# Optimization experiments

Measured on AMD Instinct MI355X. Metric: run time of the kernel, lower is better.

Reference implementation:

```python
import jax, jax.numpy as jnp
import numpy as np

H = 8  # num_heads
NEG = -1e6  # mask fill value used by the torch masked_softmax


def layernorm(x, g, b, eps=1e-5):
    mu = jnp.mean(x, axis=-1, keepdims=True)
    var = jnp.mean(jnp.square(x - mu), axis=-1, keepdims=True)
    return (x - mu) * jax.lax.rsqrt(var + eps) * g + b


def setup_inputs() -> dict:
    key = jax.random.key(0)
    ks = jax.random.split(key, 10)
    B, S, D, F = 8, 1024, 512, 2048
    s = 0.02
    return {
        "X": jax.random.normal(ks[0], (B, S, D), jnp.float32),
        "valid_lens": jax.random.randint(ks[1], (B,), 1, S + 1, jnp.int32),
        "ln1_g": jnp.ones((D,), jnp.float32),
        "ln1_b": jnp.zeros((D,), jnp.float32),
        "Wq": jax.random.normal(ks[2], (D, D), jnp.float32) * s,
        "Wk": jax.random.normal(ks[3], (D, D), jnp.float32) * s,
        "Wv": jax.random.normal(ks[4], (D, D), jnp.float32) * s,
        "Wo": jax.random.normal(ks[5], (D, D), jnp.float32) * s,
        "ln2_g": jnp.ones((D,), jnp.float32),
        "ln2_b": jnp.zeros((D,), jnp.float32),
        "W1": jax.random.normal(ks[6], (D, F), jnp.float32) * s,
        "b1": jnp.zeros((F,), jnp.float32),
        "W2": jax.random.normal(ks[7], (F, D), jnp.float32) * s,
        "b2": jnp.zeros((D,), jnp.float32),
    }


def vit_block(X, valid_lens, ln1_g, ln1_b, Wq, Wk, Wv, Wo, ln2_g, ln2_b, W1, b1, W2, b2):
    B, S, D = X.shape
    dh = D // H
    h = layernorm(X, ln1_g, ln1_b)
    # project and split heads: [B, S, H, dh]
    q = (h @ Wq).reshape(B, S, H, dh)
    k = (h @ Wk).reshape(B, S, H, dh)
    v = (h @ Wv).reshape(B, S, H, dh)
    scores = jnp.einsum("bqhd,bkhd->bhqk", q, k) / jnp.sqrt(jnp.float32(dh))
    # mask keys >= valid_len[b] with -1e6 (as in masked_softmax)
    mask = jnp.arange(S)[None, None, None, :] < valid_lens[:, None, None, None]
    scores = jnp.where(mask, scores, NEG)
    attn = jax.nn.softmax(scores, axis=-1)
    out = jnp.einsum("bhqk,bkhd->bqhd", attn, v).reshape(B, S, D)
    X = X + out @ Wo
    h2 = layernorm(X, ln2_g, ln2_b)
    mlp = jax.nn.gelu(h2 @ W1 + b1, approximate=False) @ W2 + b2
    return X + mlp


def reference(X, valid_lens, ln1_g, ln1_b, Wq, Wk, Wv, Wo, ln2_g, ln2_b, W1, b1, W2, b2):
    return vit_block(X, valid_lens, ln1_g, ln1_b, Wq, Wk, Wv, Wo, ln2_g, ln2_b, W1, b1, W2, b2)
```

## Files before the change

kernel.cpp:

```cpp
#include <hip/hip_runtime.h>
#include <math.h>

#define BB 8
#define SS 1024
#define DD 512
#define FF 2048
#define NH 8
#define MM (BB * SS)
#define LDQKV 1536

using bf8 = __attribute__((ext_vector_type(8))) short;
using f4  = __attribute__((ext_vector_type(4))) float;

#define AS1 __attribute__((address_space(1)))
#define AS3 __attribute__((address_space(3)))

__device__ __forceinline__ void gload16(const void* g, void* l) {
  __builtin_amdgcn_global_load_lds((AS1 const void*)g, (AS3 void*)l, 16, 0, 0);
}

template <int N> __device__ __forceinline__ void wait_vm() {
  if constexpr (N == 0)      asm volatile("s_waitcnt vmcnt(0)" ::: "memory");
  else if constexpr (N == 3) asm volatile("s_waitcnt vmcnt(3)" ::: "memory");
  else if constexpr (N == 4) asm volatile("s_waitcnt vmcnt(4)" ::: "memory");
  else if constexpr (N == 6) asm volatile("s_waitcnt vmcnt(6)" ::: "memory");
  else                       asm volatile("s_waitcnt vmcnt(8)" ::: "memory");
  __builtin_amdgcn_sched_barrier(0);
}

__device__ __forceinline__ void bar() {
  __builtin_amdgcn_sched_barrier(0);
  __builtin_amdgcn_s_barrier();
  __builtin_amdgcn_sched_barrier(0);
}

__device__ __forceinline__ unsigned short f2b(float f) {
  union { float f; unsigned u; } v; v.f = f;
  unsigned r = v.u + 0x7fffu + ((v.u >> 16) & 1u);
  return (unsigned short)(r >> 16);
}

__device__ __forceinline__ float gelu_f(float x) {
  float ax = fabsf(x) * 0.70710678118654752f;
  float t = 1.0f / (1.0f + 0.3275911f * ax);
  float poly = t * (0.254829592f +
               t * (-0.284496736f +
               t * (1.421413741f +
               t * (-1.453152027f + t * 1.061405429f))));
  float erfv = 1.0f - poly * __expf(-ax * ax);
  erfv = copysignf(erfv, x);
  return 0.5f * x * (1.0f + erfv);
}

__global__ __launch_bounds__(256) void ln_bf16(const float* __restrict__ x,
                                               const float* __restrict__ g,
                                               const float* __restrict__ bta,
                                               unsigned short* __restrict__ out) {
  int wave = threadIdx.x >> 6, lane = threadIdx.x & 63;
  int row = (blockIdx.x << 2) + wave;
  const float* xr = x + (size_t)row * DD;
  int base = lane << 3;
  float4 v0 = *(const float4*)(xr + base);
  float4 v1 = *(const float4*)(xr + base + 4);
  float s  = v0.x + v0.y + v0.z + v0.w + v1.x + v1.y + v1.z + v1.w;
  float sq = v0.x*v0.x + v0.y*v0.y + v0.z*v0.z + v0.w*v0.w
           + v1.x*v1.x + v1.y*v1.y + v1.z*v1.z + v1.w*v1.w;
  for (int m = 32; m; m >>= 1) { s += __shfl_xor(s, m); sq += __shfl_xor(sq, m); }
  float mu  = s * (1.0f / DD);
  float var = sq * (1.0f / DD) - mu * mu;
  float rs  = rsqrtf(var + 1e-5f);
  float xv[8], go[8], bo[8];
  *(float4*)(xv) = v0; *(float4*)(xv + 4) = v1;
  *(float4*)(go)     = *(const float4*)(g + base);
  *(float4*)(go + 4) = *(const float4*)(g + base + 4);
  *(float4*)(bo)     = *(const float4*)(bta + base);
  *(float4*)(bo + 4) = *(const float4*)(bta + base + 4);
  union { unsigned short u[8]; uint4 v; } ov;
#pragma unroll
  for (int i = 0; i < 8; i++) ov.u[i] = f2b((xv[i] - mu) * rs * go[i] + bo[i]);
  *(uint4*)(out + (size_t)row * DD + base) = ov.v;
}

__global__ __launch_bounds__(256) void tconv(const float* __restrict__ in,
                                             unsigned short* __restrict__ outp,
                                             int K, int N) {
  __shared__ float tile[32][33];
  int n0 = blockIdx.x << 5, k0 = blockIdx.y << 5;
  int c = threadIdx.x & 31, r = threadIdx.x >> 5;
#pragma unroll
  for (int i = 0; i < 4; i++)
    tile[r + 8 * i][c] = in[(size_t)(k0 + r + 8 * i) * N + n0 + c];
  __syncthreads();
#pragma unroll
  for (int i = 0; i < 4; i++)
    outp[(size_t)(n0 + r + 8 * i) * K + k0 + c] = f2b(tile[c][r + 8 * i]);
}

__global__ __launch_bounds__(256) void tconv4(
    const float* __restrict__ s0, const float* __restrict__ s1,
    const float* __restrict__ s2, const float* __restrict__ s3,
    unsigned short* __restrict__ d0, unsigned short* __restrict__ d1,
    unsigned short* __restrict__ d2, unsigned short* __restrict__ d3) {
  __shared__ float tile[32][33];
  const float* in; unsigned short* outp;
  switch (blockIdx.z) {
    case 0: in = s0; outp = d0; break;
    case 1: in = s1; outp = d1; break;
    case 2: in = s2; outp = d2; break;
    default: in = s3; outp = d3; break;
  }
  int n0 = blockIdx.x << 5, k0 = blockIdx.y << 5;
  int c = threadIdx.x & 31, r = threadIdx.x >> 5;
#pragma unroll
  for (int i = 0; i < 4; i++)
    tile[r + 8 * i][c] = in[(size_t)(k0 + r + 8 * i) * DD + n0 + c];
  __syncthreads();
#pragma unroll
  for (int i = 0; i < 4; i++)
    outp[(size_t)(n0 + r + 8 * i) * DD + k0 + c] = f2b(tile[c][r + 8 * i]);
}

template <int BM, int BN, int ACT>
__global__ __launch_bounds__(256, 4) void gemm_t(
    const unsigned short* __restrict__ A,
    const unsigned short* __restrict__ Bt,
    const float* __restrict__ bias,
    const float* __restrict__ res,
    float* __restrict__ Cf,
    unsigned short* __restrict__ Cb,
    int M, int N, int K, int gx) {
  constexpr int WM = BM / 2, WN = BN / 2;
  constexpr int FM = WM / 16, FN = WN / 16;
  constexpr int ACH = BM / 64, BCH = BN / 64;
  constexpr int L = ACH + BCH;
  __shared__ unsigned short As[2][BM * 32];
  __shared__ unsigned short Bs[2][BN * 32];
  int tid = threadIdx.x, wid = tid >> 6, lane = tid & 63;

  int bid = blockIdx.x;
  int cpx = (int)gridDim.x >> 3;
  int swz = (bid & 7) * cpx + (bid >> 3);
  int m0 = (swz / gx) * BM, n0 = (swz % gx) * BN;

  int wm = (wid >> 1) * WM, wn = (wid & 1) * WN;
  int r4 = lane & 15, ksl = lane >> 4;
  int srow = lane >> 2;
  int gs = (lane & 3) ^ ((lane >> 3) & 3);

  const unsigned short* aBase =
      A + (size_t)(m0 + wid * (ACH * 16) + srow) * K + gs * 8;
  const unsigned short* bBase =
      Bt + (size_t)(n0 + wid * (BCH * 16) + srow) * K + gs * 8;

  f4 acc[FN][FM];
#pragma unroll
  for (int i = 0; i < FN; i++)
#pragma unroll
    for (int j = 0; j < FM; j++) acc[i][j] = (f4){0.f, 0.f, 0.f, 0.f};

  auto STAGE = [&](int buf, int t) {
    int k0 = t << 5;
#pragma unroll
    for (int i = 0; i < ACH; i++)
      gload16(aBase + (size_t)i * 16 * K + k0, &As[buf][(wid * ACH + i) * 512]);
#pragma unroll
    for (int i = 0; i < BCH; i++)
      gload16(bBase + (size_t)i * 16 * K + k0, &Bs[buf][(wid * BCH + i) * 512]);
  };

  auto COMPUTE = [&](int buf) {
    bf8 af[FM], bfr[FN];
#pragma unroll
    for (int mi = 0; mi < FM; mi++) {
      int r = wm + mi * 16 + r4;
      af[mi] = *(const bf8*)((const char*)&As[buf][0] + r * 64 +
                             ((ksl ^ ((r >> 1) & 3)) << 4));
    }
#pragma unroll
    for (int ni = 0; ni < FN; ni++) {
      int r = wn + ni * 16 + r4;
      bfr[ni] = *(const bf8*)((const char*)&Bs[buf][0] + r * 64 +
                              ((ksl ^ ((r >> 1) & 3)) << 4));
    }
#pragma unroll
    for (int ni = 0; ni < FN; ni++)
#pragma unroll
      for (int mi = 0; mi < FM; mi++)
        acc[ni][mi] = __builtin_amdgcn_mfma_f32_16x16x32_bf16(
            bfr[ni], af[mi], acc[ni][mi], 0, 0, 0);
  };

  int nt = K >> 5;
  STAGE(0, 0);
  STAGE(1, 1);
  for (int t = 0; t < nt; t++) {
    if (t + 1 < nt) wait_vm<L>();
    else            wait_vm<0>();
    bar();
    COMPUTE(t & 1);
    bar();
    if (t + 2 < nt) STAGE(t & 1, t + 2);
  }

  int rq = (lane >> 4) << 2;
#pragma unroll
  for (int ni = 0; ni < FN; ni++) {
    int col = n0 + wn + ni * 16 + rq;
    float bv[4] = {0.f, 0.f, 0.f, 0.f};
    if (bias) *(float4*)bv = *(const float4*)(bias + col);
#pragma unroll
    for (int mi = 0; mi < FM; mi++) {
      int row = m0 + wm + mi * 16 + r4;
      float v[4];
#pragma unroll
      for (int j = 0; j < 4; j++) {
        v[j] = acc[ni][mi][j] + bv[j];
        if (ACT) v[j] = gelu_f(v[j]);
      }
      if (res) {
        float4 rv = *(const float4*)(res + (size_t)row * N + col);
        v[0] += rv.x; v[1] += rv.y; v[2] += rv.z; v[3] += rv.w;
      }
      if (Cf) {
        *(float4*)(Cf + (size_t)row * N + col) = *(float4*)v;
      } else {
        union { unsigned short u[4]; uint2 q; } p;
#pragma unroll
        for (int j = 0; j < 4; j++) p.u[j] = f2b(v[j]);
        *(uint2*)(Cb + (size_t)row * N + col) = p.q;
      }
    }
  }
}

__global__ __launch_bounds__(256) void attn_mfma(
    const unsigned short* __restrict__ QKV,
    const int* __restrict__ vlen,
    unsigned short* __restrict__ AO) {
  __shared__ unsigned short Qs[64 * 64];
  __shared__ unsigned short Ks[64 * 64];
  __shared__ unsigned short Vt[64 * 64];
  __shared__ unsigned short Ps[64 * 64];
  int b = blockIdx.z, h = blockIdx.y, q0 = blockIdx.x << 6;
  int tid = threadIdx.x, wid = tid >> 6, lane = tid & 63;
  int vl = vlen[b];
  int r4 = lane & 15, ksl = lane >> 4;

  int srow = lane >> 3;
  int gs = (lane & 7) ^ srow;
  {
    const unsigned short* qsrc =
        QKV + (size_t)(b * SS + q0 + wid * 16 + srow) * LDQKV + h * 64 + gs * 8;
    gload16(qsrc, Qs + wid * 1024);
    gload16(qsrc + (size_t)8 * LDQKV, Qs + wid * 1024 + 512);
  }
  const unsigned short* kbase =
      QKV + (size_t)(b * SS + wid * 16 + srow) * LDQKV + DD + h * 64 + gs * 8;
  int vp = tid & 31, vdg = (tid >> 5) << 3;
  const unsigned short* vbase =
      QKV + (size_t)(b * SS + 2 * vp) * LDQKV + 2 * DD + h * 64 + vdg;

  f4 o[4];
#pragma unroll
  for (int i = 0; i < 4; i++) o[i] = (f4){0.f, 0.f, 0.f, 0.f};
  float mrun[4], lrun[4];
#pragma unroll
  for (int j = 0; j < 4; j++) { mrun[j] = -3e38f; lrun[j] = 0.0f; }

  int ntiles = (vl + 63) >> 6;
  if (ntiles > 16) ntiles = 16;

  for (int t = 0; t < ntiles; t++) {
    int kg0 = t << 6;
    const unsigned short* ks = kbase + (size_t)kg0 * LDQKV;
    gload16(ks, Ks + wid * 1024);
    gload16(ks + (size_t)8 * LDQKV, Ks + wid * 1024 + 512);
    {
      const unsigned short* v0 = vbase + (size_t)kg0 * LDQKV;
      const unsigned short* v1 = v0 + LDQKV;
      unsigned short va[8], vb[8];
      *(uint4*)va = *(const uint4*)v0;
      *(uint4*)vb = *(const uint4*)v1;
#pragma unroll
      for (int i = 0; i < 8; i++) {
        int d = vdg + i;
        unsigned val = (unsigned)va[i] | ((unsigned)vb[i] << 16);
        int byte = (d << 7) + (((vp >> 2) ^ (d & 7)) << 4) + ((vp & 3) << 2);
        *(unsigned*)((char*)Vt + byte) = val;
      }
    }
    __syncthreads();

    f4 s[4];
#pragma unroll
    for (int i = 0; i < 4; i++) s[i] = (f4){0.f, 0.f, 0.f, 0.f};
#pragma unroll
    for (int k2 = 0; k2 < 2; k2++) {
      int slot = (k2 << 2) + ksl;
      int qr = (wid << 4) + r4;
      bf8 aq = *(const bf8*)((const char*)Qs + (qr << 7) + ((slot ^ (qr & 7)) << 4));
#pragma unroll
      for (int ni = 0; ni < 4; ni++) {
        int kr = (ni << 4) + r4;
        bf8 bk = *(const bf8*)((const char*)Ks + (kr << 7) + ((slot ^ (kr & 7)) << 4));
        s[ni] = __builtin_amdgcn_mfma_f32_16x16x32_bf16(aq, bk, s[ni], 0, 0, 0);
      }
    }

#pragma unroll
    for (int j = 0; j < 4; j++) {
      int qr = (wid << 4) + ((lane >> 4) << 2) + j;
      float sv[4], mx = -3e38f;
#pragma unroll
      for (int ni = 0; ni < 4; ni++) {
        float v = s[ni][j] * 0.125f;
        if (kg0 + (ni << 4) + r4 >= vl) v = -1e6f;
        sv[ni] = v;
        mx = fmaxf(mx, v);
      }
#pragma unroll
      for (int m2 = 1; m2 < 16; m2 <<= 1) mx = fmaxf(mx, __shfl_xor(mx, m2));
      float mnew = fmaxf(mrun[j], mx);
      float al = __expf(mrun[j] - mnew);
      float ls = 0.0f;
      unsigned short pb[4];
#pragma unroll
      for (int ni = 0; ni < 4; ni++) {
        float p = __expf(sv[ni] - mnew);
        ls += p;
        pb[ni] = f2b(p);
      }
#pragma unroll
      for (int m2 = 1; m2 < 16; m2 <<= 1) ls += __shfl_xor(ls, m2);
      lrun[j] = lrun[j] * al + ls;
      mrun[j] = mnew;
#pragma unroll
      for (int ni = 0; ni < 4; ni++) {
        int kc = (ni << 4) + r4;
        int byte = (qr << 7) + (((kc >> 3) ^ (qr & 7)) << 4) + ((kc & 7) << 1);
        *(unsigned short*)((char*)Ps + byte) = pb[ni];
        o[ni][j] *= al;
      }
    }

#pragma unroll
    for (int k2 = 0; k2 < 2; k2++) {
      int slot = (k2 << 2) + ksl;
      int qr = (wid << 4) + r4;
      bf8 ap = *(const bf8*)((const char*)Ps + (qr << 7) + ((slot ^ (qr & 7)) << 4));
#pragma unroll
      for (int ni = 0; ni < 4; ni++) {
        int dr = (ni << 4) + r4;
        bf8 bv = *(const bf8*)((const char*)Vt + (dr << 7) + ((slot ^ (dr & 7)) << 4));
        o[ni] = __builtin_amdgcn_mfma_f32_16x16x32_bf16(ap, bv, o[ni], 0, 0, 0);
      }
    }
    __syncthreads();
  }

  float inv[4];
#pragma unroll
  for (int j = 0; j < 4; j++) inv[j] = 1.0f / lrun[j];
#pragma unroll
  for (int ni = 0; ni < 4; ni++) {
#pragma unroll
    for (int j = 0; j < 4; j++) {
      int qr = (wid << 4) + ((lane >> 4) << 2) + j;
      int d = (ni << 4) + r4;
      AO[(size_t)(b * SS + q0 + qr) * DD + h * 64 + d] = f2b(o[ni][j] * inv[j]);
    }
  }
}

extern "C" void kernel_launch(void* const* d_in, const int* in_sizes, int n_in,
                              void* d_out, int out_size, void* d_ws,
                              size_t ws_size, hipStream_t stream) {
  const float* X    = (const float*)d_in[0];
  const int*   vln  = (const int*)d_in[1];
  const float* ln1g = (const float*)d_in[2];
  const float* ln1b = (const float*)d_in[3];
  const float* Wq   = (const float*)d_in[4];
  const float* Wk   = (const float*)d_in[5];
  const float* Wv   = (const float*)d_in[6];
  const float* Wo   = (const float*)d_in[7];
  const float* ln2g = (const float*)d_in[8];
  const float* ln2b = (const float*)d_in[9];
  const float* W1   = (const float*)d_in[10];
  const float* b1   = (const float*)d_in[11];
  const float* W2   = (const float*)d_in[12];
  const float* b2   = (const float*)d_in[13];
  float* out = (float*)d_out;

  unsigned short* ws = (unsigned short*)d_ws;
  unsigned short* h     = ws;
  unsigned short* QKVb  = h     + (size_t)MM * DD;
  unsigned short* AOb   = QKVb  + (size_t)MM * LDQKV;
  unsigned short* mid   = AOb   + (size_t)MM * DD;
  unsigned short* Wqkvt = mid   + (size_t)MM * FF;
  unsigned short* Wot   = Wqkvt + (size_t)3 * DD * DD;
  unsigned short* W1t   = Wot   + (size_t)DD * DD;
  unsigned short* W2t   = W1t   + (size_t)FF * DD;

  dim3 blk(256);

  tconv4<<<dim3(16, 16, 4), blk, 0, stream>>>(
      Wq, Wk, Wv, Wo, Wqkvt, Wqkvt + (size_t)DD * DD,
      Wqkvt + (size_t)2 * DD * DD, Wot);
  tconv<<<dim3(64, 16), blk, 0, stream>>>(W1, W1t, DD, FF);
  tconv<<<dim3(16, 64), blk, 0, stream>>>(W2, W2t, FF, DD);

  ln_bf16<<<dim3(MM / 4), blk, 0, stream>>>(X, ln1g, ln1b, h);
  gemm_t<128, 128, 0><<<dim3((LDQKV / 128) * (MM / 128)), blk, 0, stream>>>(
      h, Wqkvt, nullptr, nullptr, nullptr, QKVb, MM, LDQKV, DD, LDQKV / 128);
  attn_mfma<<<dim3(SS / 64, NH, BB), blk, 0, stream>>>(QKVb, vln, AOb);
  gemm_t<128, 64, 0><<<dim3((DD / 64) * (MM / 128)), blk, 0, stream>>>(
      AOb, Wot, nullptr, X, out, nullptr, MM, DD, DD, DD / 64);
  ln_bf16<<<dim3(MM / 4), blk, 0, stream>>>(out, ln2g, ln2b, h);
  gemm_t<128, 128, 1><<<dim3((FF / 128) * (MM / 128)), blk, 0, stream>>>(
      h, W1t, b1, nullptr, nullptr, mid, MM, FF, DD, FF / 128);
  gemm_t<128, 64, 0><<<dim3((DD / 64) * (MM / 128)), blk, 0, stream>>>(
      mid, W2t, b2, out, out, nullptr, MM, DD, FF, DD / 64);
}
```

Before: 179.4 us.

## Replace GEMM kernel with 512-thread 256-wide tiles and 64-deep K steps

Rewrites the bf16 MFMA GEMM to use 8 waves per block, larger output tiles (256x256 for QKV and W1, 64x256 for the D-output GEMMs) and a K step of 64 with a new 128-byte-row XOR swizzle in LDS. It also raises wave priority around the MFMA section. The goal is more data reuse per LDS load and fewer barriers per K. The trade-offs are more LDS and registers per block, lower occupancy, and fewer blocks in the grid (for example 192 for QKV), which may underfill the CUs. The epilogue changes from vectorized float4 stores to scalar per-element stores with a transposed accumulator mapping, which may reduce store coalescing.

```diff
diff --git a/kernel.cpp b/kernel.cpp
--- a/kernel.cpp
+++ b/kernel.cpp
@@ -21,10 +21,9 @@
 
 template <int N> __device__ __forceinline__ void wait_vm() {
   if constexpr (N == 0)      asm volatile("s_waitcnt vmcnt(0)" ::: "memory");
-  else if constexpr (N == 3) asm volatile("s_waitcnt vmcnt(3)" ::: "memory");
-  else if constexpr (N == 4) asm volatile("s_waitcnt vmcnt(4)" ::: "memory");
-  else if constexpr (N == 6) asm volatile("s_waitcnt vmcnt(6)" ::: "memory");
-  else                       asm volatile("s_waitcnt vmcnt(8)" ::: "memory");
+  else if constexpr (N == 5) asm volatile("s_waitcnt vmcnt(5)" ::: "memory");
+  else if constexpr (N == 8) asm volatile("s_waitcnt vmcnt(8)" ::: "memory");
+  else                       asm volatile("s_waitcnt vmcnt(16)" ::: "memory");
   __builtin_amdgcn_sched_barrier(0);
 }
 
@@ -120,8 +119,8 @@
     outp[(size_t)(n0 + r + 8 * i) * DD + k0 + c] = f2b(tile[c][r + 8 * i]);
 }
 
-template <int BM, int BN, int ACT>
-__global__ __launch_bounds__(256, 4) void gemm_t(
+template <int BM, int BN, int ACT, int MINW>
+__global__ __launch_bounds__(512, MINW) void gemm8(
     const unsigned short* __restrict__ A,
     const unsigned short* __restrict__ Bt,
     const float* __restrict__ bias,
@@ -129,12 +128,12 @@
     float* __restrict__ Cf,
     unsigned short* __restrict__ Cb,
     int M, int N, int K, int gx) {
-  constexpr int WM = BM / 2, WN = BN / 2;
+  constexpr int WM = BM / 2, WN = BN / 4;
   constexpr int FM = WM / 16, FN = WN / 16;
-  constexpr int ACH = BM / 64, BCH = BN / 64;
-  constexpr int L = ACH + BCH;
-  __shared__ unsigned short As[2][BM * 32];
-  __shared__ unsigned short Bs[2][BN * 32];
+  constexpr int ACH = BM / 8;
+  constexpr int CPW = (BM + BN) / 64;
+  __shared__ unsigned short As[2][BM * 64];
+  __shared__ unsigned short Bs[2][BN * 64];
   int tid = threadIdx.x, wid = tid >> 6, lane = tid & 63;
 
   int bid = blockIdx.x;
@@ -142,59 +141,69 @@
   int swz = (bid & 7) * cpx + (bid >> 3);
   int m0 = (swz / gx) * BM, n0 = (swz % gx) * BN;
 
-  int wm = (wid >> 1) * WM, wn = (wid & 1) * WN;
+  int wm = (wid >> 2) * WM, wn = (wid & 3) * WN;
   int r4 = lane & 15, ksl = lane >> 4;
-  int srow = lane >> 2;
-  int gs = (lane & 3) ^ ((lane >> 3) & 3);
-
-  const unsigned short* aBase =
-      A + (size_t)(m0 + wid * (ACH * 16) + srow) * K + gs * 8;
-  const unsigned short* bBase =
-      Bt + (size_t)(n0 + wid * (BCH * 16) + srow) * K + gs * 8;
-
-  f4 acc[FN][FM];
-#pragma unroll
-  for (int i = 0; i < FN; i++)
-#pragma unroll
-    for (int j = 0; j < FM; j++) acc[i][j] = (f4){0.f, 0.f, 0.f, 0.f};
+  int srow = lane >> 3;
+  int gs = (lane & 7) ^ srow;
+
+  f4 acc[FM][FN];
+#pragma unroll
+  for (int i = 0; i < FM; i++)
+#pragma unroll
+    for (int j = 0; j < FN; j++) acc[i][j] = (f4){0.f, 0.f, 0.f, 0.f};
 
   auto STAGE = [&](int buf, int t) {
-    int k0 = t << 5;
-#pragma unroll
-    for (int i = 0; i < ACH; i++)
-      gload16(aBase + (size_t)i * 16 * K + k0, &As[buf][(wid * ACH + i) * 512]);
-#pragma unroll
-    for (int i = 0; i < BCH; i++)
-      gload16(bBase + (size_t)i * 16 * K + k0, &Bs[buf][(wid * BCH + i) * 512]);
+    int k0 = t << 6;
+#pragma unroll
+    for (int i = 0; i < CPW; i++) {
+      int c = wid * CPW + i;
+      const unsigned short* src;
+      unsigned short* dst;
+      if (c < ACH) {
+        src = A + (size_t)(m0 + c * 8 + srow) * K + k0 + gs * 8;
+        dst = &As[buf][c * 512];
+      } else {
+        int c2 = c - ACH;
+        src = Bt + (size_t)(n0 + c2 * 8 + srow) * K + k0 + gs * 8;
+        dst = &Bs[buf][c2 * 512];
+      }
+      gload16(src, dst);
+    }
   };
 
   auto COMPUTE = [&](int buf) {
-    bf8 af[FM], bfr[FN];
-#pragma unroll
-    for (int mi = 0; mi < FM; mi++) {
-      int r = wm + mi * 16 + r4;
-      af[mi] = *(const bf8*)((const char*)&As[buf][0] + r * 64 +
-                             ((ksl ^ ((r >> 1) & 3)) << 4));
-    }
-#pragma unroll
-    for (int ni = 0; ni < FN; ni++) {
-      int r = wn + ni * 16 + r4;
-      bfr[ni] = *(const bf8*)((const char*)&Bs[buf][0] + r * 64 +
-                              ((ksl ^ ((r >> 1) & 3)) << 4));
-    }
-#pragma unroll
-    for (int ni = 0; ni < FN; ni++)
+    __builtin_amdgcn_s_setprio(1);
+#pragma unroll
+    for (int k2 = 0; k2 < 2; k2++) {
+      int slot = (k2 << 2) | ksl;
+      bf8 af[FM], bfr[FN];
+#pragma unroll
+      for (int mi = 0; mi < FM; mi++) {
+        int r = wm + mi * 16 + r4;
+        af[mi] = *(const bf8*)((const char*)&As[buf][0] + r * 128 +
+                               ((slot ^ (r & 7)) << 4));
+      }
+#pragma unroll
+      for (int ni = 0; ni < FN; ni++) {
+        int r = wn + ni * 16 + r4;
+        bfr[ni] = *(const bf8*)((const char*)&Bs[buf][0] + r * 128 +
+                                ((slot ^ (r & 7)) << 4));
+      }
 #pragma unroll
       for (int mi = 0; mi < FM; mi++)
-        acc[ni][mi] = __builtin_amdgcn_mfma_f32_16x16x32_bf16(
-            bfr[ni], af[mi], acc[ni][mi], 0, 0, 0);
+#pragma unroll
+        for (int ni = 0; ni < FN; ni++)
+          acc[mi][ni] = __builtin_amdgcn_mfma_f32_16x16x32_bf16(
+              af[mi], bfr[ni], acc[mi][ni], 0, 0, 0);
+    }
+    __builtin_amdgcn_s_setprio(0);
   };
 
-  int nt = K >> 5;
+  int nt = K >> 6;
   STAGE(0, 0);
   STAGE(1, 1);
   for (int t = 0; t < nt; t++) {
-    if (t + 1 < nt) wait_vm<L>();
+    if (t + 1 < nt) wait_vm<CPW>();
     else            wait_vm<0>();
     bar();
     COMPUTE(t & 1);
@@ -205,29 +214,18 @@
   int rq = (lane >> 4) << 2;
 #pragma unroll
   for (int ni = 0; ni < FN; ni++) {
-    int col = n0 + wn + ni * 16 + rq;
-    float bv[4] = {0.f, 0.f, 0.f, 0.f};
-    if (bias) *(float4*)bv = *(const float4*)(bias + col);
+    int col = n0 + wn + ni * 16 + r4;
+    float bv = bias ? bias[col] : 0.0f;
 #pragma unroll
     for (int mi = 0; mi < FM; mi++) {
-      int row = m0 + wm + mi * 16 + r4;
-      float v[4];
 #pragma unroll
       for (int j = 0; j < 4; j++) {
-        v[j] = acc[ni][mi][j] + bv[j];
-        if (ACT) v[j] = gelu_f(v[j]);
-      }
-      if (res) {
-        float4 rv = *(const float4*)(res + (size_t)row * N + col);
-        v[0] += rv.x; v[1] += rv.y; v[2] += rv.z; v[3] += rv.w;
-      }
-      if (Cf) {
-        *(float4*)(Cf + (size_t)row * N + col) = *(float4*)v;
-      } else {
-        union { unsigned short u[4]; uint2 q; } p;
-#pragma unroll
-        for (int j = 0; j < 4; j++) p.u[j] = f2b(v[j]);
-        *(uint2*)(Cb + (size_t)row * N + col) = p.q;
+        int row = m0 + wm + mi * 16 + rq + j;
+        float v = acc[mi][ni][j] + bv;
+        if (ACT) v = gelu_f(v);
+        if (res) v += res[(size_t)row * N + col];
+        if (Cf) Cf[(size_t)row * N + col] = v;
+        else    Cb[(size_t)row * N + col] = f2b(v);
       }
     }
   }
@@ -402,6 +400,7 @@
   unsigned short* W2t   = W1t   + (size_t)FF * DD;
 
   dim3 blk(256);
+  dim3 blk8(512);
 
   tconv4<<<dim3(16, 16, 4), blk, 0, stream>>>(
       Wq, Wk, Wv, Wo, Wqkvt, Wqkvt + (size_t)DD * DD,
@@ -410,14 +409,14 @@
   tconv<<<dim3(16, 64), blk, 0, stream>>>(W2, W2t, FF, DD);
 
   ln_bf16<<<dim3(MM / 4), blk, 0, stream>>>(X, ln1g, ln1b, h);
-  gemm_t<128, 128, 0><<<dim3((LDQKV / 128) * (MM / 128)), blk, 0, stream>>>(
-      h, Wqkvt, nullptr, nullptr, nullptr, QKVb, MM, LDQKV, DD, LDQKV / 128);
+  gemm8<256, 256, 0, 2><<<dim3((LDQKV / 256) * (MM / 256)), blk8, 0, stream>>>(
+      h, Wqkvt, nullptr, nullptr, nullptr, QKVb, MM, LDQKV, DD, LDQKV / 256);
   attn_mfma<<<dim3(SS / 64, NH, BB), blk, 0, stream>>>(QKVb, vln, AOb);
-  gemm_t<128, 64, 0><<<dim3((DD / 64) * (MM / 128)), blk, 0, stream>>>(
-      AOb, Wot, nullptr, X, out, nullptr, MM, DD, DD, DD / 64);
+  gemm8<64, 256, 0, 4><<<dim3((DD / 256) * (MM / 64)), blk8, 0, stream>>>(
+      AOb, Wot, nullptr, X, out, nullptr, MM, DD, DD, DD / 256);
   ln_bf16<<<dim3(MM / 4), blk, 0, stream>>>(out, ln2g, ln2b, h);
-  gemm_t<128, 128, 1><<<dim3((FF / 128) * (MM / 128)), blk, 0, stream>>>(
-      h, W1t, b1, nullptr, nullptr, mid, MM, FF, DD, FF / 128);
-  gemm_t<128, 64, 0><<<dim3((DD / 64) * (MM / 128)), blk, 0, stream>>>(
-      mid, W2t, b2, out, out, nullptr, MM, DD, FF, DD / 64);
-}
+  gemm8<256, 256, 1, 2><<<dim3((FF / 256) * (MM / 256)), blk8, 0, stream>>>(
+      h, W1t, b1, nullptr, nullptr, mid, MM, FF, DD, FF / 256);
+  gemm8<64, 256, 0, 4><<<dim3((DD / 256) * (MM / 64)), blk8, 0, stream>>>(
+      mid, W2t, b2, out, out, nullptr, MM, DD, FF, DD / 256);
+}
```

New measurement: 253.9 us. 1.42x slower.

## Add 256x256 8-wave GEMM for QKV and FFN1; drop LDS swizzle in gemm_t

Applied to the files above, without the earlier changes.

Adds a new 512-thread GEMM kernel with 256x256 tiles and K-step 64. It splits each K-step into four quarter-phases that interleave LDS fragment loads, global prefetch and MFMA groups under raised wave priority, and it is used for the QKV projection and the first MLP layer. The goal is more data reuse per tile and better overlap of loads with compute. The generic gemm_t is also changed: the XOR swizzle on LDS is removed, chunk loads are spread evenly across waves, and the epilogue switches to scalar stores. Dropping the swizzle may bring back LDS bank conflicts, the scalar stores may coalesce worse, and the large tiles produce fewer blocks, which could leave compute units idle.

```diff
diff --git a/kernel.cpp b/kernel.cpp
--- a/kernel.cpp
+++ b/kernel.cpp
@@ -23,7 +23,6 @@
   if constexpr (N == 0)      asm volatile("s_waitcnt vmcnt(0)" ::: "memory");
   else if constexpr (N == 3) asm volatile("s_waitcnt vmcnt(3)" ::: "memory");
   else if constexpr (N == 4) asm volatile("s_waitcnt vmcnt(4)" ::: "memory");
-  else if constexpr (N == 6) asm volatile("s_waitcnt vmcnt(6)" ::: "memory");
   else                       asm volatile("s_waitcnt vmcnt(8)" ::: "memory");
   __builtin_amdgcn_sched_barrier(0);
 }
@@ -31,6 +30,11 @@
 __device__ __forceinline__ void bar() {
   __builtin_amdgcn_sched_barrier(0);
   __builtin_amdgcn_s_barrier();
+  __builtin_amdgcn_sched_barrier(0);
+}
+
+__device__ __forceinline__ void lgk0() {
+  asm volatile("s_waitcnt lgkmcnt(0)" ::: "memory");
   __builtin_amdgcn_sched_barrier(0);
 }
 
@@ -120,6 +124,141 @@
     outp[(size_t)(n0 + r + 8 * i) * DD + k0 + c] = f2b(tile[c][r + 8 * i]);
 }
 
+#define MQ256(g, g2)                                                         \
+  do {                                                                       \
+    __builtin_amdgcn_s_setprio(1);                                           \
+    _Pragma("unroll") for (int mi = 0; mi < 4; mi++)                         \
+      _Pragma("unroll") for (int u = 0; u < 2; u++)                          \
+        _Pragma("unroll") for (int k2 = 0; k2 < 2; k2++)                     \
+          acc[(g) * 4 + mi][(g2) * 2 + u] =                                  \
+              __builtin_amdgcn_mfma_f32_16x16x32_bf16(                       \
+                  af[mi][k2], bfr[(g2) * 2 + u][k2],                         \
+                  acc[(g) * 4 + mi][(g2) * 2 + u], 0, 0, 0);                 \
+    __builtin_amdgcn_s_setprio(0);                                           \
+  } while (0)
+
+#define LB256(g2, buf)                                                       \
+  do {                                                                       \
+    _Pragma("unroll") for (int u = 0; u < 2; u++) {                          \
+      int r = rb + ((g2) * 2 + u) * 16 + r4;                                 \
+      _Pragma("unroll") for (int k2 = 0; k2 < 2; k2++)                       \
+        bfr[(g2) * 2 + u][k2] = *(const bf8*)((const char*)Bs[buf][hb] +     \
+            r * 128 + ((((k2 << 2) | ksl) ^ (r & 7)) << 4));                 \
+    }                                                                        \
+  } while (0)
+
+template <int ACT>
+__global__ __launch_bounds__(512, 1) void gemm256(
+    const unsigned short* __restrict__ A,
+    const unsigned short* __restrict__ Bt,
+    const float* __restrict__ bias,
+    unsigned short* __restrict__ Cb,
+    int M, int N, int K, int gx) {
+  __shared__ unsigned short As[2][2][128 * 64];
+  __shared__ unsigned short Bs[2][2][128 * 64];
+  int tid = threadIdx.x, wid = tid >> 6, lane = tid & 63;
+
+  int bid = blockIdx.x, cpx = (int)gridDim.x >> 3;
+  int swz = (bid & 7) * cpx + (bid >> 3);
+  int m0 = (swz / gx) << 8, n0 = (swz % gx) << 8;
+
+  int wm = (wid >> 2) << 7;
+  int wn = (wid & 3) << 6;
+  int ha = wm >> 7, hb = wn >> 7, rb = wn & 64;
+  int r4 = lane & 15, ksl = lane >> 4;
+  int srow = lane >> 3, gs = (lane & 7) ^ srow;
+
+  f4 acc[8][4];
+#pragma unroll
+  for (int i = 0; i < 8; i++)
+#pragma unroll
+    for (int j = 0; j < 4; j++) acc[i][j] = (f4){0.f, 0.f, 0.f, 0.f};
+  bf8 af[4][2], bfr[4][2];
+
+  auto SA = [&](int h, int t) {
+    int buf = t & 1, k0 = t << 6;
+#pragma unroll
+    for (int i = 0; i < 2; i++) {
+      int ch = wid * 2 + i;
+      gload16(A + (size_t)(m0 + h * 128 + ch * 8 + srow) * K + k0 + gs * 8,
+              &As[buf][h][ch * 512]);
+    }
+  };
+  auto SB = [&](int h, int t) {
+    int buf = t & 1, k0 = t << 6;
+#pragma unroll
+    for (int i = 0; i < 2; i++) {
+      int ch = wid * 2 + i;
+      gload16(Bt + (size_t)(n0 + h * 128 + ch * 8 + srow) * K + k0 + gs * 8,
+              &Bs[buf][h][ch * 512]);
+    }
+  };
+  auto LA = [&](int g, int buf) {
+#pragma unroll
+    for (int mi = 0; mi < 4; mi++) {
+      int r = g * 64 + mi * 16 + r4;
+#pragma unroll
+      for (int k2 = 0; k2 < 2; k2++)
+        af[mi][k2] = *(const bf8*)((const char*)As[buf][ha] + r * 128 +
+                                   ((((k2 << 2) | ksl) ^ (r & 7)) << 4));
+    }
+  };
+
+  int nt = K >> 6;
+  SB(0, 0); SB(1, 0); SA(0, 0); SA(1, 0); SB(0, 1); SB(1, 1);
+  wait_vm<4>();
+  bar();
+
+  for (int T = 0; T < nt; T++) {
+    int buf = T & 1;
+    LA(0, buf);
+    LB256(0, buf);
+    if (T + 1 < nt) SA(0, T + 1);
+    bar(); lgk0();
+    MQ256(0, 0);
+    bar();
+    LB256(1, buf);
+    if (T + 1 < nt) SA(1, T + 1);
+    bar(); lgk0();
+    MQ256(0, 1);
+    bar();
+    LA(1, buf);
+    if (T + 2 < nt) SB(0, T + 2);
+    bar(); lgk0();
+    MQ256(1, 0);
+    bar();
+    if (T + 2 < nt) SB(1, T + 2);
+    bar(); lgk0();
+    MQ256(1, 1);
+    if (T + 1 < nt) {
+      if (T + 2 < nt) wait_vm<4>();
+      else            wait_vm<0>();
+    }
+    bar();
+  }
+  wait_vm<0>();
+
+  int rq = ksl << 2;
+  float bv[4];
+#pragma unroll
+  for (int ni = 0; ni < 4; ni++)
+    bv[ni] = bias ? bias[n0 + wn + ni * 16 + r4] : 0.0f;
+#pragma unroll
+  for (int mi = 0; mi < 8; mi++) {
+#pragma unroll
+    for (int j = 0; j < 4; j++) {
+      int row = m0 + wm + mi * 16 + rq + j;
+#pragma unroll
+      for (int ni = 0; ni < 4; ni++) {
+        int col = n0 + wn + ni * 16 + r4;
+        float v = acc[mi][ni][j] + bv[ni];
+        if (ACT) v = gelu_f(v);
+        Cb[(size_t)row * N + col] = f2b(v);
+      }
+    }
+  }
+}
+
 template <int BM, int BN, int ACT>
 __global__ __launch_bounds__(256, 4) void gemm_t(
     const unsigned short* __restrict__ A,
@@ -131,63 +270,59 @@
     int M, int N, int K, int gx) {
   constexpr int WM = BM / 2, WN = BN / 2;
   constexpr int FM = WM / 16, FN = WN / 16;
-  constexpr int ACH = BM / 64, BCH = BN / 64;
-  constexpr int L = ACH + BCH;
+  constexpr int NCHA = BM / 16;
+  constexpr int NCH = (BM + BN) / 16;
+  constexpr int L = NCH / 4;
   __shared__ unsigned short As[2][BM * 32];
   __shared__ unsigned short Bs[2][BN * 32];
   int tid = threadIdx.x, wid = tid >> 6, lane = tid & 63;
 
-  int bid = blockIdx.x;
-  int cpx = (int)gridDim.x >> 3;
+  int bid = blockIdx.x, cpx = (int)gridDim.x >> 3;
   int swz = (bid & 7) * cpx + (bid >> 3);
   int m0 = (swz / gx) * BM, n0 = (swz % gx) * BN;
 
   int wm = (wid >> 1) * WM, wn = (wid & 1) * WN;
   int r4 = lane & 15, ksl = lane >> 4;
-  int srow = lane >> 2;
-  int gs = (lane & 3) ^ ((lane >> 3) & 3);
-
-  const unsigned short* aBase =
-      A + (size_t)(m0 + wid * (ACH * 16) + srow) * K + gs * 8;
-  const unsigned short* bBase =
-      Bt + (size_t)(n0 + wid * (BCH * 16) + srow) * K + gs * 8;
-
-  f4 acc[FN][FM];
-#pragma unroll
-  for (int i = 0; i < FN; i++)
-#pragma unroll
-    for (int j = 0; j < FM; j++) acc[i][j] = (f4){0.f, 0.f, 0.f, 0.f};
+  int srow = lane >> 2, gs = lane & 3;
+
+  f4 acc[FM][FN];
+#pragma unroll
+  for (int i = 0; i < FM; i++)
+#pragma unroll
+    for (int j = 0; j < FN; j++) acc[i][j] = (f4){0.f, 0.f, 0.f, 0.f};
 
   auto STAGE = [&](int buf, int t) {
     int k0 = t << 5;
 #pragma unroll
-    for (int i = 0; i < ACH; i++)
-      gload16(aBase + (size_t)i * 16 * K + k0, &As[buf][(wid * ACH + i) * 512]);
-#pragma unroll
-    for (int i = 0; i < BCH; i++)
-      gload16(bBase + (size_t)i * 16 * K + k0, &Bs[buf][(wid * BCH + i) * 512]);
+    for (int i = 0; i < L; i++) {
+      int c = wid * L + i;
+      if (c < NCHA)
+        gload16(A + (size_t)(m0 + c * 16 + srow) * K + k0 + gs * 8,
+                &As[buf][c * 512]);
+      else
+        gload16(Bt + (size_t)(n0 + (c - NCHA) * 16 + srow) * K + k0 + gs * 8,
+                &Bs[buf][(c - NCHA) * 512]);
+    }
   };
 
   auto COMPUTE = [&](int buf) {
     bf8 af[FM], bfr[FN];
 #pragma unroll
-    for (int mi = 0; mi < FM; mi++) {
-      int r = wm + mi * 16 + r4;
-      af[mi] = *(const bf8*)((const char*)&As[buf][0] + r * 64 +
-                             ((ksl ^ ((r >> 1) & 3)) << 4));
-    }
-#pragma unroll
-    for (int ni = 0; ni < FN; ni++) {
-      int r = wn + ni * 16 + r4;
-      bfr[ni] = *(const bf8*)((const char*)&Bs[buf][0] + r * 64 +
-                              ((ksl ^ ((r >> 1) & 3)) << 4));
-    }
+    for (int mi = 0; mi < FM; mi++)
+      af[mi] = *(const bf8*)((const char*)&As[buf][0] +
+                             (wm + mi * 16 + r4) * 64 + ksl * 16);
 #pragma unroll
     for (int ni = 0; ni < FN; ni++)
-#pragma unroll
-      for (int mi = 0; mi < FM; mi++)
-        acc[ni][mi] = __builtin_amdgcn_mfma_f32_16x16x32_bf16(
-            bfr[ni], af[mi], acc[ni][mi], 0, 0, 0);
+      bfr[ni] = *(const bf8*)((const char*)&Bs[buf][0] +
+                              (wn + ni * 16 + r4) * 64 + ksl * 16);
+    __builtin_amdgcn_s_setprio(1);
+#pragma unroll
+    for (int mi = 0; mi < FM; mi++)
+#pragma unroll
+      for (int ni = 0; ni < FN; ni++)
+        acc[mi][ni] = __builtin_amdgcn_mfma_f32_16x16x32_bf16(
+            af[mi], bfr[ni], acc[mi][ni], 0, 0, 0);
+    __builtin_amdgcn_s_setprio(0);
   };
 
   int nt = K >> 5;
@@ -202,32 +337,24 @@
     if (t + 2 < nt) STAGE(t & 1, t + 2);
   }
 
-  int rq = (lane >> 4) << 2;
-#pragma unroll
-  for (int ni = 0; ni < FN; ni++) {
-    int col = n0 + wn + ni * 16 + rq;
-    float bv[4] = {0.f, 0.f, 0.f, 0.f};
-    if (bias) *(float4*)bv = *(const float4*)(bias + col);
-#pragma unroll
-    for (int mi = 0; mi < FM; mi++) {
-      int row = m0 + wm + mi * 16 + r4;
-      float v[4];
-#pragma unroll
-      for (int j = 0; j < 4; j++) {
-        v[j] = acc[ni][mi][j] + bv[j];
-        if (ACT) v[j] = gelu_f(v[j]);
-      }
-      if (res) {
-        float4 rv = *(const float4*)(res + (size_t)row * N + col);
-        v[0] += rv.x; v[1] += rv.y; v[2] += rv.z; v[3] += rv.w;
-      }
-      if (Cf) {
-        *(float4*)(Cf + (size_t)row * N + col) = *(float4*)v;
-      } else {
-        union { unsigned short u[4]; uint2 q; } p;
-#pragma unroll
-        for (int j = 0; j < 4; j++) p.u[j] = f2b(v[j]);
-        *(uint2*)(Cb + (size_t)row * N + col) = p.q;
+  int rq = ksl << 2;
+  float bv[FN];
+#pragma unroll
+  for (int ni = 0; ni < FN; ni++)
+    bv[ni] = bias ? bias[n0 + wn + ni * 16 + r4] : 0.0f;
+#pragma unroll
+  for (int mi = 0; mi < FM; mi++) {
+#pragma unroll
+    for (int j = 0; j < 4; j++) {
+      int row = m0 + wm + mi * 16 + rq + j;
+#pragma unroll
+      for (int ni = 0; ni < FN; ni++) {
+        int col = n0 + wn + ni * 16 + r4;
+        float v = acc[mi][ni][j] + bv[ni];
+        if (ACT) v = gelu_f(v);
+        if (res) v += res[(size_t)row * N + col];
+        if (Cf) Cf[(size_t)row * N + col] = v;
+        else    Cb[(size_t)row * N + col] = f2b(v);
       }
     }
   }
@@ -402,6 +529,7 @@
   unsigned short* W2t   = W1t   + (size_t)FF * DD;
 
   dim3 blk(256);
+  dim3 blk8(512);
 
   tconv4<<<dim3(16, 16, 4), blk, 0, stream>>>(
       Wq, Wk, Wv, Wo, Wqkvt, Wqkvt + (size_t)DD * DD,
@@ -410,14 +538,14 @@
   tconv<<<dim3(16, 64), blk, 0, stream>>>(W2, W2t, FF, DD);
 
   ln_bf16<<<dim3(MM / 4), blk, 0, stream>>>(X, ln1g, ln1b, h);
-  gemm_t<128, 128, 0><<<dim3((LDQKV / 128) * (MM / 128)), blk, 0, stream>>>(
-      h, Wqkvt, nullptr, nullptr, nullptr, QKVb, MM, LDQKV, DD, LDQKV / 128);
+  gemm256<0><<<dim3((LDQKV / 256) * (MM / 256)), blk8, 0, stream>>>(
+      h, Wqkvt, nullptr, QKVb, MM, LDQKV, DD, LDQKV / 256);
   attn_mfma<<<dim3(SS / 64, NH, BB), blk, 0, stream>>>(QKVb, vln, AOb);
   gemm_t<128, 64, 0><<<dim3((DD / 64) * (MM / 128)), blk, 0, stream>>>(
       AOb, Wot, nullptr, X, out, nullptr, MM, DD, DD, DD / 64);
   ln_bf16<<<dim3(MM / 4), blk, 0, stream>>>(out, ln2g, ln2b, h);
-  gemm_t<128, 128, 1><<<dim3((FF / 128) * (MM / 128)), blk, 0, stream>>>(
-      h, W1t, b1, nullptr, nullptr, mid, MM, FF, DD, FF / 128);
+  gemm256<1><<<dim3((FF / 256) * (MM / 256)), blk8, 0, stream>>>(
+      h, W1t, b1, mid, MM, FF, DD, FF / 256);
   gemm_t<128, 64, 0><<<dim3((DD / 64) * (MM / 128)), blk, 0, stream>>>(
       mid, W2t, b2, out, out, nullptr, MM, DD, FF, DD / 64);
 }
```

After: 180.3 us. About the same (+0.5%).
